# Kernel tuning notes

Hardware: AMD Instinct MI355X
Metric: run time of the kernel (lower is better)

## Reference

```python
import jax, jax.numpy as jnp
import numpy as np

TEMP = 0.05
MOM = 0.2
B, D = 256, 768
NI, NC = 65536, 8192
T = 128
K, RATE = 50, 38


def _l2norm(x):
    return x / jnp.linalg.norm(x, axis=-1, keepdims=True)


def _ce_target0(logits):
    # cross-entropy where the correct class is column 0
    return jnp.mean(jax.nn.logsumexp(logits, axis=1) - logits[:, 0])


def setup_inputs() -> dict:
    key = jax.random.key(0)
    ks = jax.random.split(key, 8)
    inputs = jax.random.normal(ks[0], (B, D), dtype=jnp.float32)
    cls_tok = jax.random.normal(ks[1], (B, D), dtype=jnp.float32)
    part_tok = jax.random.normal(ks[2], (B, D), dtype=jnp.float32)
    tokens = jax.random.normal(ks[3], (B, T, D), dtype=jnp.float32)
    mem_features = _l2norm(jax.random.normal(ks[4], (NI, D), dtype=jnp.float32))
    cluster_features = _l2norm(jax.random.normal(ks[5], (NC, D), dtype=jnp.float32))
    targets = jax.random.randint(ks[6], (B,), 0, NC, dtype=jnp.int32)
    # unique instance indexes (each batch sample owns a distinct memory slot)
    indexes = jax.random.permutation(ks[7], NI)[:B].astype(jnp.int32)
    # every cluster label appears in the instance memory -> positives always exist
    mem_labels = (jnp.arange(NI, dtype=jnp.int32) % NC)
    return {
        "inputs": inputs, "cls_tok": cls_tok, "part_tok": part_tok,
        "tokens": tokens, "mem_features": mem_features,
        "cluster_features": cluster_features, "targets": targets,
        "indexes": indexes, "mem_labels": mem_labels, "k": K, "rate": RATE,
    }


def reference(inputs, cls_tok, part_tok, tokens, mem_features, cluster_features,
              targets, indexes, mem_labels, k, rate):
    x = _l2norm(inputs)  # F.normalize(inputs, dim=1)

    # ---- patch_refine: (cls.tokens + part.tokens)/2, sort, hardest pos / easiest negs
    mat_p = 0.5 * (jnp.einsum('bd,btd->bt', cls_tok, tokens)
                   + jnp.einsum('bd,btd->bt', part_tok, tokens))  # [B, T]
    s = jnp.sort(mat_p, axis=1)  # ascending
    patch_logits = jnp.concatenate([s[:, -1:], s[:, :rate]], axis=1) / TEMP  # [B, 1+rate]
    patch_loss = _ce_target0(patch_logits)

    # ---- anchor: detached instance memory, hardest positive + top-k hardest negatives
    mem = jax.lax.stop_gradient(mem_features)          # features.clone().detach()
    mat = x @ mem.T                                     # [B, NI]
    pos_mask = mem_labels[None, :] == targets[:, None]  # [B, NI]
    pos = jnp.min(jnp.where(pos_mask, mat, jnp.inf), axis=1)          # argmin over positives
    negs, _ = jax.lax.top_k(jnp.where(pos_mask, -jnp.inf, mat), k)    # sorted desc top-k negs
    anchor_logits = jnp.concatenate([pos[:, None], negs], axis=1) / TEMP  # [B, 1+k]
    anchor_loss = _ce_target0(anchor_logits)

    # ---- cm_hard forward: inputs @ cluster_features.T (custom Fn: no grad to features)
    logits = (x @ jax.lax.stop_gradient(cluster_features).T) / TEMP  # [B, NC]
    lse = jax.nn.logsumexp(logits, axis=1)
    tgt_logit = jnp.take_along_axis(logits, targets[:, None].astype(jnp.int32), axis=1)[:, 0]
    cluster_loss = jnp.mean(lse - tgt_logit)

    loss = cluster_loss + anchor_loss + patch_loss

    # ---- momentum scatter-update of instance memory (torch.no_grad block)
    xs = jax.lax.stop_gradient(x)
    upd = MOM * mem[indexes] + (1.0 - MOM) * xs  # [B, D]
    upd = _l2norm(upd)
    new_mem = mem.at[indexes].set(upd)

    return loss, new_mem
```

## Files before the change

### kernel.cpp

```cpp
#include <hip/hip_runtime.h>
#include <hip/hip_bf16.h>

#define B_    256
#define D_    768
#define NI_   65536
#define NC_   8192
#define TT_   128
#define KK_   50
#define RATE_ 38
#define NBIN_ 4096

#define TOTF_  ((long)NI_ * D_)
#define NCH_   (TOTF_ / 8)

#define PBLK_   256
#define NMEMT_  (NI_ / 128 * 2)
#define NCLUT_  (NC_ / 128 * 2)

constexpr float INVT_ = 20.0f;
constexpr float MOM_  = 0.2f;

typedef __attribute__((ext_vector_type(8))) short          bf16x8;
typedef __attribute__((ext_vector_type(8))) unsigned short u16x8;
typedef __attribute__((ext_vector_type(4))) float          f32x4;

static __device__ __forceinline__ unsigned short f2bf(float f) {
    unsigned int u = __builtin_bit_cast(unsigned int, f);
    unsigned int r = u + 0x7fffu + ((u >> 16) & 1u);
    return (unsigned short)(r >> 16);
}
static __device__ __forceinline__ float bf2f(unsigned short u) {
    return __builtin_bit_cast(float, (unsigned int)u << 16);
}
static __device__ __forceinline__ unsigned int pack2(float x, float y) {
    return (unsigned int)f2bf(x) | ((unsigned int)f2bf(y) << 16);
}
static __device__ __forceinline__ int val2bin(float v) {
    int bin = (int)((v + 1.0f) * (float)(NBIN_ / 2));
    return bin < 0 ? 0 : (bin > NBIN_ - 1 ? NBIN_ - 1 : bin);
}
static __device__ __forceinline__ void glds16(const void* g, void* l) {
    __builtin_amdgcn_global_load_lds(
        (const __attribute__((address_space(1))) void*)g,
        (__attribute__((address_space(3))) void*)l, 16, 0, 0);
}

__global__ __launch_bounds__(256) void k_norm_x(const float* __restrict__ in,
                                                float* __restrict__ xf,
                                                unsigned short* __restrict__ xb,
                                                unsigned int* __restrict__ ghist) {
    int b = blockIdx.x, t = threadIdx.x;
    {
        int base = (b * 256 + t) * 16;
#pragma unroll
        for (int i = 0; i < 16; i++) ghist[base + i] = 0u;
    }
    __shared__ float red[256];
    float v[3]; float ss = 0.f;
#pragma unroll
    for (int i = 0; i < 3; i++) { v[i] = in[b * D_ + t + 256 * i]; ss += v[i] * v[i]; }
    red[t] = ss; __syncthreads();
    for (int s = 128; s > 0; s >>= 1) { if (t < s) red[t] += red[t + s]; __syncthreads(); }
    float rn = 1.0f / sqrtf(red[0]);
#pragma unroll
    for (int i = 0; i < 3; i++) {
        float x = v[i] * rn;
        xf[b * D_ + t + 256 * i] = x;
        xb[b * D_ + t + 256 * i] = f2bf(x);
    }
}

__global__ __launch_bounds__(256) void k_stream(const float* __restrict__ src,
                                                float* __restrict__ dst) {
    long gid = (long)blockIdx.x * blockDim.x + threadIdx.x;
    const long stride = (long)gridDim.x * blockDim.x;
    for (long k = gid; k < NCH_ - 1; k += stride) {
        const long s = k * 8;
        f32x4 a0 = *(const f32x4*)(src + s);
        f32x4 a1 = *(const f32x4*)(src + s + 4);
        f32x4 c0 = *(const f32x4*)(src + s + 8);
        f32x4 w0 = {a0.w, a1.x, a1.y, a1.z};
        f32x4 w1 = {a1.w, c0.x, c0.y, c0.z};
        __builtin_nontemporal_store(w0, (f32x4*)(dst + s + 3));
        __builtin_nontemporal_store(w1, (f32x4*)(dst + s + 7));
    }
    if (gid == 0) {
        for (int i = 0; i < 3; i++) __builtin_nontemporal_store(src[i], dst + i);
        const long s = TOTF_ - 8;
        for (int i = 3; i < 8; i++) __builtin_nontemporal_store(src[s + i], dst + s + i);
    }
}

__global__ __launch_bounds__(256) void k_gemm(const unsigned short* __restrict__ A,
                                              const float* __restrict__ memf,
                                              const float* __restrict__ clusf,
                                              unsigned short* __restrict__ mat,
                                              unsigned short* __restrict__ clog,
                                              const float* __restrict__ cls,
                                              const float* __restrict__ part,
                                              const float* __restrict__ tok,
                                              float* __restrict__ patchL) {
    __shared__ __align__(16) char SMEM[24576];
    const int tid = threadIdx.x;
    const int bx = blockIdx.x;

    if (bx < PBLK_) {
        float* s  = (float*)SMEM;
        float* pp = s + D_;
        float* mp = pp + 256;
        int b = bx, t = tid;
        int tt = t & 127, h = t >> 7;
        for (int i = t; i < D_; i += 256) s[i] = 0.5f * (cls[b * D_ + i] + part[b * D_ + i]);
        __syncthreads();
        const float* tr = tok + ((long)b * TT_ + tt) * D_ + h * 384;
        const float* sh = s + h * 384;
        float acc = 0.f;
#pragma unroll 8
        for (int d = 0; d < 384; d += 4) {
            float4 tv = *(const float4*)(tr + d);
            float4 sv = *(const float4*)(sh + d);
            acc += tv.x * sv.x + tv.y * sv.y + tv.z * sv.z + tv.w * sv.w;
        }
        pp[t] = acc; __syncthreads();
        if (t < TT_) mp[t] = pp[t] + pp[t + 128];
        __syncthreads();
        for (int k = 2; k <= TT_; k <<= 1)
            for (int j = k >> 1; j > 0; j >>= 1) {
                if (t < TT_) {
                    int ixj = t ^ j;
                    if (ixj > t) {
                        float a = mp[t], c = mp[ixj];
                        bool up = ((t & k) == 0);
                        if ((a > c) == up) { mp[t] = c; mp[ixj] = a; }
                    }
                }
                __syncthreads();
            }
        if (t == 0) {
            float m = mp[TT_ - 1];
            float sum = 0.f;
            for (int i = 0; i < RATE_; i++) sum += expf((mp[i] - m) * INVT_);
            patchL[b] = log1pf(sum);
        }
        return;
    }

    unsigned short* As = (unsigned short*)SMEM;
    float*          Bs = (float*)(SMEM + 8192);

    const int lane = tid & 63, w = tid >> 6;
    const int wm = w >> 1, wn = w & 1;
    const int rl = lane & 15, kg = lane >> 4;

    const float* Bsrc; unsigned short* C; int N; int tIdx;
    if (bx < PBLK_ + NMEMT_) { Bsrc = memf;  C = mat;  N = NI_; tIdx = bx - PBLK_; }
    else                     { Bsrc = clusf; C = clog; N = NC_; tIdx = bx - PBLK_ - NMEMT_; }
    const int n0 = (tIdx >> 1) * 128;
    const int m0 = (tIdx & 1) * 128;

    const unsigned short* gA0 = A + (m0 + (w * 2) * 16 + (lane >> 2)) * D_ + (lane & 3) * 8;
    const float*          gB0 = Bsrc + (long)(n0 + (w * 4) * 8 + (lane >> 3)) * D_ + (lane & 7) * 4;

    f32x4 acc[4][4] = {};

    for (int k0 = 0; k0 < D_; k0 += 32) {
        glds16(gA0 + k0,            (char*)As + (w * 2) * 1024);
        glds16(gA0 + 16 * D_ + k0,  (char*)As + (w * 2 + 1) * 1024);
#pragma unroll
        for (int ii = 0; ii < 4; ii++)
            glds16(gB0 + ii * 8 * D_ + k0, (char*)Bs + (w * 4 + ii) * 1024);
        __syncthreads();

        bf16x8 af[4];
#pragma unroll
        for (int i = 0; i < 4; i++)
            af[i] = *(const bf16x8*)((const char*)As + ((wm * 64 + i * 16 + rl) * 64 + kg * 16));
        uint4 bw[4];
#pragma unroll
        for (int j = 0; j < 4; j++) {
            const float* bp = (const float*)((const char*)Bs + ((wn * 64 + j * 16 + rl) * 128 + kg * 32));
            float4 lo = *(const float4*)bp;
            float4 hi = *(const float4*)(bp + 4);
            bw[j].x = pack2(lo.x, lo.y); bw[j].y = pack2(lo.z, lo.w);
            bw[j].z = pack2(hi.x, hi.y); bw[j].w = pack2(hi.z, hi.w);
        }
#pragma unroll
        for (int i = 0; i < 4; i++)
#pragma unroll
            for (int j = 0; j < 4; j++)
                acc[i][j] = __builtin_amdgcn_mfma_f32_16x16x32_bf16(
                    af[i], __builtin_bit_cast(bf16x8, bw[j]), acc[i][j], 0, 0, 0);
        __syncthreads();
    }

#pragma unroll
    for (int i = 0; i < 4; i++)
#pragma unroll
        for (int j = 0; j < 4; j++) {
            int col = n0 + wn * 64 + j * 16 + rl;
#pragma unroll
            for (int r = 0; r < 4; r++) {
                int row = m0 + wm * 64 + i * 16 + kg * 4 + r;
                C[(long)row * N + col] = f2bf(acc[i][j][r]);
            }
        }
}

__global__ __launch_bounds__(256) void k_cluster(const unsigned short* __restrict__ clog,
                                                 const int* __restrict__ targets,
                                                 float* __restrict__ clusterL) {
    int b = blockIdx.x, t = threadIdx.x;
    __shared__ float red[256];
    const u16x8* row = (const u16x8*)(clog + (long)b * NC_);
    float mx = -1e30f;
#pragma unroll
    for (int i = t; i < NC_ / 8; i += 256) {
        u16x8 v = row[i];
#pragma unroll
        for (int e = 0; e < 8; e++) mx = fmaxf(mx, bf2f(v[e]));
    }
    red[t] = mx; __syncthreads();
    for (int s = 128; s > 0; s >>= 1) { if (t < s) red[t] = fmaxf(red[t], red[t + s]); __syncthreads(); }
    mx = red[0]; __syncthreads();
    float sum = 0.f;
#pragma unroll
    for (int i = t; i < NC_ / 8; i += 256) {
        u16x8 v = row[i];
#pragma unroll
        for (int e = 0; e < 8; e++) sum += expf((bf2f(v[e]) - mx) * INVT_);
    }
    red[t] = sum; __syncthreads();
    for (int s = 128; s > 0; s >>= 1) { if (t < s) red[t] += red[t + s]; __syncthreads(); }
    if (t == 0) {
        float lse = mx * INVT_ + logf(red[0]);
        clusterL[b] = lse - bf2f(clog[(long)b * NC_ + targets[b]]) * INVT_;
    }
}

__global__ __launch_bounds__(256) void k_hist(const unsigned short* __restrict__ mat,
                                              const int* __restrict__ targets,
                                              unsigned int* __restrict__ ghist) {
    int b = blockIdx.y, ch = blockIdx.x, t = threadIdx.x;
    int tgt = targets[b];
    __shared__ unsigned int h[NBIN_];
    for (int i = t; i < NBIN_; i += 256) h[i] = 0;
    __syncthreads();
    const u16x8* row = (const u16x8*)(mat + (long)b * NI_);
#pragma unroll
    for (int j = 0; j < 4; j++) {
        int c8 = ch * 1024 + j * 256 + t;
        u16x8 v = row[c8];
        int i0 = c8 * 8;
#pragma unroll
        for (int e = 0; e < 8; e++)
            if (((i0 + e) & (NC_ - 1)) != tgt)
                atomicAdd(&h[val2bin(bf2f(v[e]))], 1u);
    }
    __syncthreads();
    unsigned int* gh = ghist + (long)b * NBIN_;
    for (int i = t; i < NBIN_; i += 256) { unsigned int c = h[i]; if (c) atomicAdd(&gh[i], c); }
}

__global__ __launch_bounds__(256) void k_scan(const unsigned int* __restrict__ ghist,
                                              int* __restrict__ tbv,
                                              unsigned int* __restrict__ gcnt) {
    int b = blockIdx.x, t = threadIdx.x;
    if (t == 0) gcnt[b] = 0;
    const unsigned int* gh = ghist + (long)b * NBIN_;
    __shared__ unsigned int s[256];
    unsigned int sum = 0;
    for (int i = 0; i < 16; i++) sum += gh[t * 16 + i];
    s[t] = sum; __syncthreads();
    for (int off = 1; off < 256; off <<= 1) {
        unsigned int v = (t + off < 256) ? s[t + off] : 0u;
        __syncthreads();
        s[t] += v; __syncthreads();
    }
    unsigned int nextv = (t < 255) ? s[t + 1] : 0u;
    if (s[t] >= KK_ && nextv < KK_) {
        unsigned int cum = nextv;
        int tb = t * 16;
        for (int bin = t * 16 + 15; bin >= t * 16; bin--) {
            cum += gh[bin];
            if (cum >= KK_) { tb = bin; break; }
        }
        tbv[b] = tb;
    }
}

__global__ __launch_bounds__(256) void k_collect(const unsigned short* __restrict__ mat,
                                                 const int* __restrict__ targets,
                                                 const int* __restrict__ tbv,
                                                 unsigned int* __restrict__ gcnt,
                                                 float* __restrict__ cand) {
    int b = blockIdx.y, ch = blockIdx.x, t = threadIdx.x;
    int tgt = targets[b];
    int tb = tbv[b];
    const u16x8* row = (const u16x8*)(mat + (long)b * NI_);
#pragma unroll
    for (int j = 0; j < 4; j++) {
        int c8 = ch * 1024 + j * 256 + t;
        u16x8 v = row[c8];
        int i0 = c8 * 8;
#pragma unroll
        for (int e = 0; e < 8; e++) {
            float f = bf2f(v[e]);
            if (((i0 + e) & (NC_ - 1)) != tgt && val2bin(f) >= tb) {
                unsigned int p = atomicAdd(&gcnt[b], 1u);
                if (p < 256) cand[b * 256 + p] = f;
            }
        }
    }
}

__global__ __launch_bounds__(256) void k_final(const unsigned short* __restrict__ mat,
                                               const int* __restrict__ targets,
                                               const unsigned int* __restrict__ gcnt,
                                               const float* __restrict__ cand,
                                               float* __restrict__ anchorL) {
    int b = blockIdx.x, t = threadIdx.x;
    int tgt = targets[b];
    __shared__ float c[256];
    __shared__ float pm[8];
    unsigned int n = gcnt[b]; if (n > 256u) n = 256u;
    c[t] = (t < (int)n) ? cand[b * 256 + t] : -1e30f;
    if (t < 8) pm[t] = bf2f(mat[(long)b * NI_ + tgt + t * NC_]);
    __syncthreads();
    for (int k = 2; k <= 256; k <<= 1)
        for (int j = k >> 1; j > 0; j >>= 1) {
            int ixj = t ^ j;
            if (ixj > t) {
                float a = c[t], d = c[ixj];
                bool down = ((t & k) == 0);
                if ((a < d) == down) { c[t] = d; c[ixj] = a; }
            }
            __syncthreads();
        }
    if (t == 0) {
        float posmin = pm[0];
        for (int i = 1; i < 8; i++) posmin = fminf(posmin, pm[i]);
        float m = fmaxf(posmin, c[0]);
        float sum = expf((posmin - m) * INVT_);
        for (int i = 0; i < KK_; i++) sum += expf((c[i] - m) * INVT_);
        anchorL[b] = m * INVT_ + logf(sum) - posmin * INVT_;
    }
}

__global__ __launch_bounds__(256) void k_update(const float* __restrict__ mem,
                                                const float* __restrict__ xf,
                                                const int* __restrict__ indexes,
                                                float* __restrict__ out_mem) {
    int b = blockIdx.x, t = threadIdx.x;
    int idx = indexes[b];
    __shared__ float red[256];
    float u[3]; float ss = 0.f;
#pragma unroll
    for (int i = 0; i < 3; i++) {
        int d = t + 256 * i;
        u[i] = MOM_ * mem[(long)idx * D_ + d] + (1.0f - MOM_) * xf[b * D_ + d];
        ss += u[i] * u[i];
    }
    red[t] = ss; __syncthreads();
    for (int s = 128; s > 0; s >>= 1) { if (t < s) red[t] += red[t + s]; __syncthreads(); }
    float rn = 1.0f / sqrtf(red[0]);
#pragma unroll
    for (int i = 0; i < 3; i++) {
        int d = t + 256 * i;
        out_mem[(long)idx * D_ + d] = u[i] * rn;
    }
}

__global__ __launch_bounds__(256) void k_loss(const float* __restrict__ pL,
                                              const float* __restrict__ aL,
                                              const float* __restrict__ cL,
                                              float* __restrict__ out) {
    int t = threadIdx.x;
    __shared__ float red[256];
    red[t] = pL[t] + aL[t] + cL[t];
    __syncthreads();
    for (int s = 128; s > 0; s >>= 1) { if (t < s) red[t] += red[t + s]; __syncthreads(); }
    if (t == 0) out[0] = red[0] / (float)B_;
}

extern "C" void kernel_launch(void* const* d_in, const int* in_sizes, int n_in,
                              void* d_out, int out_size, void* d_ws, size_t ws_size,
                              hipStream_t stream) {
    const float* inputs   = (const float*)d_in[0];
    const float* cls_tok  = (const float*)d_in[1];
    const float* part_tok = (const float*)d_in[2];
    const float* tokens   = (const float*)d_in[3];
    const float* mem_f    = (const float*)d_in[4];
    const float* clus_f   = (const float*)d_in[5];
    const int*   targets  = (const int*)d_in[6];
    const int*   indexes  = (const int*)d_in[7];

    char* ws = (char*)d_ws;
    float*          xf      = (float*)(ws);
    unsigned short* xb      = (unsigned short*)(ws + 786432);
    float*          cand    = (float*)(ws + 786432);
    unsigned int*   gcnt    = (unsigned int*)(ws + 1048576);
    int*            tbv     = (int*)(ws + 1049600);
    unsigned short* mat     = (unsigned short*)(ws + 1179648);
    unsigned short* clog    = (unsigned short*)(ws + 34734080);
    unsigned int*   ghist   = (unsigned int*)(ws + 38928384);
    float*          patchL  = (float*)(ws + 43122688);
    float*          anchorL = (float*)(ws + 43123712);
    float*          clusterL= (float*)(ws + 43124736);

    float* out   = (float*)d_out;
    float* out_f = out + 1;

    k_norm_x<<<B_, 256, 0, stream>>>(inputs, xf, xb, ghist);

    k_stream<<<2048, 256, 0, stream>>>(mem_f, out_f);

    k_gemm<<<PBLK_ + NMEMT_ + NCLUT_, 256, 0, stream>>>(
        xb, mem_f, clus_f, mat, clog, cls_tok, part_tok, tokens, patchL);

    k_cluster<<<B_, 256, 0, stream>>>(clog, targets, clusterL);

    k_hist<<<dim3(8, B_), 256, 0, stream>>>(mat, targets, ghist);
    k_scan<<<B_, 256, 0, stream>>>(ghist, tbv, gcnt);
    k_collect<<<dim3(8, B_), 256, 0, stream>>>(mat, targets, tbv, gcnt, cand);
    k_final<<<B_, 256, 0, stream>>>(mat, targets, gcnt, cand, anchorL);

    k_update<<<B_, 256, 0, stream>>>(mem_f, xf, indexes, out_f);

    k_loss<<<1, 256, 0, stream>>>(patchL, anchorL, clusterL, out);
}
```

Measured before the change: 238.7 us.

## Fuse memory copy stream into GEMM kernel with interleaved roles and full-M tiles

```diff
diff --git a/kernel.cpp b/kernel.cpp
--- a/kernel.cpp
+++ b/kernel.cpp
@@ -10,12 +10,14 @@
 #define RATE_ 38
 #define NBIN_ 4096
 
-#define TOTF_  ((long)NI_ * D_)
-#define NCH_   (TOTF_ / 8)
-
-#define PBLK_   256
-#define NMEMT_  (NI_ / 128 * 2)
-#define NCLUT_  (NC_ / 128 * 2)
+#define TOTF_   ((long)NI_ * D_)
+#define NWIN_   ((TOTF_ - 3 - 5) / 8)
+#define NWIN8_  (NWIN_ / 8)
+
+#define NCPB_   256
+#define NPB_    256
+#define NMEMT_  (NI_ / 64)
+#define NCLUT_  (NC_ / 64)
 
 constexpr float INVT_ = 20.0f;
 constexpr float MOM_  = 0.2f;
@@ -70,32 +72,12 @@
     }
 }
 
-__global__ __launch_bounds__(256) void k_stream(const float* __restrict__ src,
-                                                float* __restrict__ dst) {
-    long gid = (long)blockIdx.x * blockDim.x + threadIdx.x;
-    const long stride = (long)gridDim.x * blockDim.x;
-    for (long k = gid; k < NCH_ - 1; k += stride) {
-        const long s = k * 8;
-        f32x4 a0 = *(const f32x4*)(src + s);
-        f32x4 a1 = *(const f32x4*)(src + s + 4);
-        f32x4 c0 = *(const f32x4*)(src + s + 8);
-        f32x4 w0 = {a0.w, a1.x, a1.y, a1.z};
-        f32x4 w1 = {a1.w, c0.x, c0.y, c0.z};
-        __builtin_nontemporal_store(w0, (f32x4*)(dst + s + 3));
-        __builtin_nontemporal_store(w1, (f32x4*)(dst + s + 7));
-    }
-    if (gid == 0) {
-        for (int i = 0; i < 3; i++) __builtin_nontemporal_store(src[i], dst + i);
-        const long s = TOTF_ - 8;
-        for (int i = 3; i < 8; i++) __builtin_nontemporal_store(src[s + i], dst + s + i);
-    }
-}
-
-__global__ __launch_bounds__(256) void k_gemm(const unsigned short* __restrict__ A,
+__global__ __launch_bounds__(256) void k_mega(const unsigned short* __restrict__ A,
                                               const float* __restrict__ memf,
                                               const float* __restrict__ clusf,
                                               unsigned short* __restrict__ mat,
                                               unsigned short* __restrict__ clog,
+                                              float* __restrict__ out_f,
                                               const float* __restrict__ cls,
                                               const float* __restrict__ part,
                                               const float* __restrict__ tok,
@@ -104,11 +86,40 @@
     const int tid = threadIdx.x;
     const int bx = blockIdx.x;
 
-    if (bx < PBLK_) {
+    int role, rid;
+    if (bx < 1536) {
+        int s6 = bx % 6, q6 = bx / 6;
+        if (s6 == 0)      { role = 0; rid = q6; }
+        else if (s6 == 3) { role = 1; rid = q6; }
+        else              { role = 2; rid = q6 * 4 + (s6 < 3 ? s6 - 1 : s6 - 2); }
+    } else { role = 3; rid = bx - 1536; }
+
+    if (role == 0) {
+        long k8 = (long)rid * 256 + tid;
+        for (; k8 < NWIN8_; k8 += (long)NCPB_ * 256) {
+            const long s = k8 * 64;
+            f32x4 v[17];
+#pragma unroll
+            for (int i = 0; i < 17; i++) v[i] = *(const f32x4*)(memf + s + i * 4);
+#pragma unroll
+            for (int i = 0; i < 16; i++) {
+                f32x4 w = {v[i].w, v[i + 1].x, v[i + 1].y, v[i + 1].z};
+                __builtin_nontemporal_store(w, (f32x4*)(out_f + s + 3 + i * 4));
+            }
+        }
+        if (rid == 0 && tid == 0) {
+            for (int i = 0; i < 3; i++) __builtin_nontemporal_store(memf[i], out_f + i);
+            for (long i = NWIN8_ * 64 + 3; i < TOTF_; i++)
+                __builtin_nontemporal_store(memf[i], out_f + i);
+        }
+        return;
+    }
+
+    if (role == 1) {
         float* s  = (float*)SMEM;
         float* pp = s + D_;
         float* mp = pp + 256;
-        int b = bx, t = tid;
+        int b = rid, t = tid;
         int tt = t & 127, h = t >> 7;
         for (int i = t; i < D_; i += 256) s[i] = 0.5f * (cls[b * D_ + i] + part[b * D_ + i]);
         __syncthreads();
@@ -146,43 +157,47 @@
     }
 
     unsigned short* As = (unsigned short*)SMEM;
-    float*          Bs = (float*)(SMEM + 8192);
+    float*          Bs = (float*)(SMEM + 16384);
 
     const int lane = tid & 63, w = tid >> 6;
-    const int wm = w >> 1, wn = w & 1;
     const int rl = lane & 15, kg = lane >> 4;
 
-    const float* Bsrc; unsigned short* C; int N; int tIdx;
-    if (bx < PBLK_ + NMEMT_) { Bsrc = memf;  C = mat;  N = NI_; tIdx = bx - PBLK_; }
-    else                     { Bsrc = clusf; C = clog; N = NC_; tIdx = bx - PBLK_ - NMEMT_; }
-    const int n0 = (tIdx >> 1) * 128;
-    const int m0 = (tIdx & 1) * 128;
-
-    const unsigned short* gA0 = A + (m0 + (w * 2) * 16 + (lane >> 2)) * D_ + (lane & 3) * 8;
-    const float*          gB0 = Bsrc + (long)(n0 + (w * 4) * 8 + (lane >> 3)) * D_ + (lane & 7) * 4;
+    const float* Bsrc; unsigned short* C; int N; int n0;
+    if (role == 2) { Bsrc = memf;  C = mat;  N = NI_; n0 = rid * 64; }
+    else           { Bsrc = clusf; C = clog; N = NC_; n0 = rid * 64; }
+
+    const unsigned short* gA = A + (w * 64 + (lane >> 2)) * D_
+                                 + (((lane & 3) ^ ((lane >> 2) & 3)) * 8);
+    const float* gB = Bsrc + (long)(n0 + w * 16 + (lane >> 3)) * D_
+                           + (((lane & 7) ^ (lane >> 3)) * 4);
+
+    const int aslot = (kg ^ (rl & 3)) * 16;
+    const int p0s   = ((kg * 2) ^ (rl & 7)) * 16;
+    const int p1s   = p0s ^ 16;
 
     f32x4 acc[4][4] = {};
 
     for (int k0 = 0; k0 < D_; k0 += 32) {
-        glds16(gA0 + k0,            (char*)As + (w * 2) * 1024);
-        glds16(gA0 + 16 * D_ + k0,  (char*)As + (w * 2 + 1) * 1024);
 #pragma unroll
         for (int ii = 0; ii < 4; ii++)
-            glds16(gB0 + ii * 8 * D_ + k0, (char*)Bs + (w * 4 + ii) * 1024);
+            glds16(gA + ii * 16 * D_ + k0, (char*)As + w * 4096 + ii * 1024);
+#pragma unroll
+        for (int ii = 0; ii < 2; ii++)
+            glds16(gB + ii * 8 * D_ + k0, (char*)Bs + w * 2048 + ii * 1024);
         __syncthreads();
 
         bf16x8 af[4];
 #pragma unroll
         for (int i = 0; i < 4; i++)
-            af[i] = *(const bf16x8*)((const char*)As + ((wm * 64 + i * 16 + rl) * 64 + kg * 16));
+            af[i] = *(const bf16x8*)((const char*)As + (w * 64 + i * 16 + rl) * 64 + aslot);
         uint4 bw[4];
 #pragma unroll
         for (int j = 0; j < 4; j++) {
-            const float* bp = (const float*)((const char*)Bs + ((wn * 64 + j * 16 + rl) * 128 + kg * 32));
-            float4 lo = *(const float4*)bp;
-            float4 hi = *(const float4*)(bp + 4);
-            bw[j].x = pack2(lo.x, lo.y); bw[j].y = pack2(lo.z, lo.w);
-            bw[j].z = pack2(hi.x, hi.y); bw[j].w = pack2(hi.z, hi.w);
+            const char* rb = (const char*)Bs + (j * 16 + rl) * 128;
+            float4 p0 = *(const float4*)(rb + p0s);
+            float4 p1 = *(const float4*)(rb + p1s);
+            bw[j].x = pack2(p0.x, p0.y); bw[j].y = pack2(p0.z, p0.w);
+            bw[j].z = pack2(p1.x, p1.y); bw[j].w = pack2(p1.z, p1.w);
         }
 #pragma unroll
         for (int i = 0; i < 4; i++)
@@ -197,10 +212,10 @@
     for (int i = 0; i < 4; i++)
 #pragma unroll
         for (int j = 0; j < 4; j++) {
-            int col = n0 + wn * 64 + j * 16 + rl;
+            int col = n0 + j * 16 + rl;
 #pragma unroll
             for (int r = 0; r < 4; r++) {
-                int row = m0 + wm * 64 + i * 16 + kg * 4 + r;
+                int row = w * 64 + i * 16 + kg * 4 + r;
                 C[(long)row * N + col] = f2bf(acc[i][j][r]);
             }
         }
@@ -412,10 +427,8 @@
 
     k_norm_x<<<B_, 256, 0, stream>>>(inputs, xf, xb, ghist);
 
-    k_stream<<<2048, 256, 0, stream>>>(mem_f, out_f);
-
-    k_gemm<<<PBLK_ + NMEMT_ + NCLUT_, 256, 0, stream>>>(
-        xb, mem_f, clus_f, mat, clog, cls_tok, part_tok, tokens, patchL);
+    k_mega<<<1536 + NCLUT_, 256, 0, stream>>>(
+        xb, mem_f, clus_f, mat, clog, out_f, cls_tok, part_tok, tokens, patchL);
 
     k_cluster<<<B_, 256, 0, stream>>>(clog, targets, clusterL);
 
```

Result: slower. 477.1 us (+99.9%).
